# Kernel tuning notes

Measured on AMD Instinct MI355X. Metric: run time of the kernel, lower is better.

Reference implementation:

```python
import jax, jax.numpy as jnp
import numpy as np


def setup_inputs() -> dict:
    key = jax.random.key(0)
    k1, k2 = jax.random.split(key)
    L = 4096000  # 160^3 mesh points
    B = 64       # receivers
    # mesh coordinates in a 10m x 8m x 3m room
    mesh_3D = jax.random.uniform(k1, (L, 3), dtype=jnp.float32) * jnp.array([10.0, 8.0, 3.0], jnp.float32)
    receiver_pos = jax.random.uniform(k2, (B, 3), dtype=jnp.float32) * jnp.array([10.0, 8.0, 3.0], jnp.float32)
    return {"mesh_3D": mesh_3D, "receiver_pos": receiver_pos}


def reference(mesh_3D, receiver_pos):
    # mesh_3D: (L, 3) flattened meshgrid; receiver_pos: (B, 3)
    mesh_flat = mesh_3D.reshape(-1, 3)                      # (L, 3)
    L = mesh_flat.shape[0]
    # Brute-force squared distances via ||m||^2 - 2 m.r + ||r||^2 -> (B, L)
    # (sqrt is monotone, argmin unchanged; distances themselves are not returned)
    m_sq = jnp.sum(mesh_flat * mesh_flat, axis=1)           # (L,)
    r_sq = jnp.sum(receiver_pos * receiver_pos, axis=1)     # (B,)
    cross = receiver_pos @ mesh_flat.T                      # (B, L)
    d2 = m_sq[None, :] - 2.0 * cross + r_sq[:, None]        # (B, L)
    min_idx = jnp.argmin(d2, axis=1)                        # (B,)
    one_hot = jnp.zeros((L,), mesh_flat.dtype).at[min_idx].set(1.0)
    closest_points = mesh_flat[min_idx]                     # (B, 3)
    input_tensor = jnp.concatenate([mesh_flat, one_hot[:, None]], axis=1)  # (L, 4)
    return input_tensor, closest_points
```

## Files before the change

### kernel.cpp

```cpp
#include <hip/hip_runtime.h>
#include <cfloat>
#include <math.h>
#include <stdint.h>

#pragma clang fp contract(off)

#define RPW 16
#define PPL 4
#define NQ  256

__device__ __forceinline__ uint32_t monotone_key(float f) {
    uint32_t u = __float_as_uint(f);
    return (u & 0x80000000u) ? ~u : (u | 0x80000000u);
}

__device__ __forceinline__ float rfl_f(float x) {
    return __uint_as_float((uint32_t)__builtin_amdgcn_readfirstlane((int)__float_as_uint(x)));
}

__global__ void __launch_bounds__(256, 4) fused_kernel(
        const float* __restrict__ mesh, const float* __restrict__ recv,
        float* __restrict__ out, unsigned long long* __restrict__ ws,
        int L, int B, int ntiles) {
    __shared__ unsigned long long lds1[256][RPW + 1];
    __shared__ unsigned long long lds2[16][RPW + 1];

    const int tid  = threadIdx.x;
    const int lane = tid & 63;
    const int wave = tid >> 6;
    const int rq   = blockIdx.x / NQ;
    const int q0   = blockIdx.x % NQ;

    float rx[RPW], ry[RPW], rz[RPW], rsq[RPW];
#pragma unroll
    for (int c = 0; c < RPW; ++c) {
        const int r = rq * RPW + c;
        float x = 0.f, y = 0.f, z = 0.f;
        if (r < B) {
            x = recv[r * 3 + 0];
            y = recv[r * 3 + 1];
            z = recv[r * 3 + 2];
        }
        rx[c]  = rfl_f(x);
        ry[c]  = rfl_f(y);
        rz[c]  = rfl_f(z);
        rsq[c] = rfl_f((x * x + y * y) + z * z);
    }

    float best[RPW];
    int   bidx[RPW];
#pragma unroll
    for (int c = 0; c < RPW; ++c) { best[c] = FLT_MAX; bidx[c] = 0x7fffffff; }

    const bool writer = (rq == 0);

    for (int t = q0; t < ntiles; t += NQ) {
        const int p0 = (t << 10) + (wave << 8) + (lane << 2);
        float xs[PPL], ys[PPL], zs[PPL], ms[PPL];
        if (p0 + PPL <= L) {
            const float4* __restrict__ m4 = (const float4*)(mesh + (size_t)p0 * 3);
            const float4 fa = m4[0], fb = m4[1], fc = m4[2];
            if (writer) {
                float4* __restrict__ o4 = (float4*)(out + (size_t)p0 * 4);
                o4[0] = make_float4(fa.x, fa.y, fa.z, 0.f);
                o4[1] = make_float4(fa.w, fb.x, fb.y, 0.f);
                o4[2] = make_float4(fb.z, fb.w, fc.x, 0.f);
                o4[3] = make_float4(fc.y, fc.z, fc.w, 0.f);
            }
            xs[0] = fa.x; ys[0] = fa.y; zs[0] = fa.z;
            xs[1] = fa.w; ys[1] = fb.x; zs[1] = fb.y;
            xs[2] = fb.z; ys[2] = fb.w; zs[2] = fc.x;
            xs[3] = fc.y; ys[3] = fc.z; zs[3] = fc.w;
#pragma unroll
            for (int j = 0; j < PPL; ++j)
                ms[j] = (xs[j] * xs[j] + ys[j] * ys[j]) + zs[j] * zs[j];
        } else {
#pragma unroll
            for (int j = 0; j < PPL; ++j) {
                const int p = p0 + j;
                if (p < L) {
                    xs[j] = mesh[(size_t)p * 3 + 0];
                    ys[j] = mesh[(size_t)p * 3 + 1];
                    zs[j] = mesh[(size_t)p * 3 + 2];
                    ms[j] = (xs[j] * xs[j] + ys[j] * ys[j]) + zs[j] * zs[j];
                    if (writer) {
                        out[(size_t)p * 4 + 0] = xs[j];
                        out[(size_t)p * 4 + 1] = ys[j];
                        out[(size_t)p * 4 + 2] = zs[j];
                        out[(size_t)p * 4 + 3] = 0.f;
                    }
                } else {
                    xs[j] = 0.f; ys[j] = 0.f; zs[j] = 0.f;
                    ms[j] = INFINITY;
                }
            }
        }
#pragma unroll
        for (int j = 0; j < PPL; ++j) {
            const int gidx = p0 + j;
#pragma unroll
            for (int c = 0; c < RPW; ++c) {
                float cr = fmaf(rz[c], zs[j], fmaf(ry[c], ys[j], rx[c] * xs[j]));
                float d2 = fmaf(-2.0f, cr, ms[j]) + rsq[c];
                if (d2 < best[c]) { best[c] = d2; bidx[c] = gidx; }
            }
        }
    }

#pragma unroll
    for (int c = 0; c < RPW; ++c)
        lds1[tid][c] = ((unsigned long long)monotone_key(best[c]) << 32)
                       | (unsigned int)bidx[c];
    __syncthreads();

    {
        const int c = tid & 15;
        const int g = tid >> 4;
        unsigned long long k = lds1[g * 16][c];
#pragma unroll
        for (int s = 1; s < 16; ++s) {
            unsigned long long o = lds1[g * 16 + s][c];
            if (o < k) k = o;
        }
        lds2[g][c] = k;
    }
    __syncthreads();

    if (tid < RPW) {
        unsigned long long k = lds2[0][tid];
#pragma unroll
        for (int p = 1; p < 16; ++p) {
            unsigned long long o = lds2[p][tid];
            if (o < k) k = o;
        }
        const int r = rq * RPW + tid;
        if (r < B) atomicMin(&ws[r], k);
    }
}

__global__ void finalize_kernel(
        const float* __restrict__ mesh, const unsigned long long* __restrict__ ws,
        float* __restrict__ out, int L, int B) {
    const int r = threadIdx.x;
    if (r >= B) return;
    const int idx = (int)(ws[r] & 0xFFFFFFFFull);
    out[(size_t)idx * 4 + 3] = 1.0f;
    float* cp = out + (size_t)L * 4 + (size_t)r * 3;
    cp[0] = mesh[(size_t)idx * 3 + 0];
    cp[1] = mesh[(size_t)idx * 3 + 1];
    cp[2] = mesh[(size_t)idx * 3 + 2];
}

extern "C" void kernel_launch(void* const* d_in, const int* in_sizes, int n_in,
                              void* d_out, int out_size, void* d_ws, size_t ws_size,
                              hipStream_t stream) {
    const float* mesh = (const float*)d_in[0];
    const float* recv = (const float*)d_in[1];
    float* out = (float*)d_out;
    const int L = in_sizes[0] / 3;
    const int B = in_sizes[1] / 3;
    unsigned long long* ws = (unsigned long long*)d_ws;

    hipMemsetAsync(ws, 0xFF, (size_t)B * sizeof(unsigned long long), stream);

    const int ntiles = (L + 1023) / 1024;
    fused_kernel<<<4 * NQ, 256, 0, stream>>>(mesh, recv, out, ws, L, B, ntiles);

    finalize_kernel<<<1, 64, 0, stream>>>(mesh, ws, out, L, B);
}
```

Baseline: 70.21 us.

## Spread output writes across receiver groups, double grid, shuffle-based block reduction

Doubles the number of tile-parallel blocks and raises the launch-bounds occupancy hint from 4 to 8 blocks per CU. The (L,4) output write is spread across all four receiver-group blocks (each writes the tiles where t mod 4 matches its group) rather than only group 0, which balances store traffic. The large LDS reduction buffer is replaced by a wave-level 64-bit shuffle reduction plus a tiny per-wave LDS array. The higher occupancy target may force register spilling, given the 16-receiver state per thread.

Measured after the change: 147.8 us. +110.6%, slower.

```diff
diff --git a/kernel.cpp b/kernel.cpp
--- a/kernel.cpp
+++ b/kernel.cpp
@@ -6,8 +6,7 @@
 #pragma clang fp contract(off)
 
 #define RPW 16
-#define PPL 4
-#define NQ  256
+#define NQ  512
 
 __device__ __forceinline__ uint32_t monotone_key(float f) {
     uint32_t u = __float_as_uint(f);
@@ -18,12 +17,18 @@
     return __uint_as_float((uint32_t)__builtin_amdgcn_readfirstlane((int)__float_as_uint(x)));
 }
 
-__global__ void __launch_bounds__(256, 4) fused_kernel(
+__device__ __forceinline__ unsigned long long shfl_xor_u64(unsigned long long v, int m) {
+    uint32_t lo = (uint32_t)v, hi = (uint32_t)(v >> 32);
+    lo = (uint32_t)__shfl_xor((int)lo, m, 64);
+    hi = (uint32_t)__shfl_xor((int)hi, m, 64);
+    return ((unsigned long long)hi << 32) | lo;
+}
+
+__global__ void __launch_bounds__(256, 8) fused_kernel(
         const float* __restrict__ mesh, const float* __restrict__ recv,
         float* __restrict__ out, unsigned long long* __restrict__ ws,
         int L, int B, int ntiles) {
-    __shared__ unsigned long long lds1[256][RPW + 1];
-    __shared__ unsigned long long lds2[16][RPW + 1];
+    __shared__ unsigned long long wmin[4][RPW];
 
     const int tid  = threadIdx.x;
     const int lane = tid & 63;
@@ -52,85 +57,67 @@
 #pragma unroll
     for (int c = 0; c < RPW; ++c) { best[c] = FLT_MAX; bidx[c] = 0x7fffffff; }
 
-    const bool writer = (rq == 0);
+    auto eval_point = [&](float x, float y, float z, int gidx) {
+        const float ms = (x * x + y * y) + z * z;
+#pragma unroll
+        for (int c = 0; c < RPW; ++c) {
+            float cr = fmaf(rz[c], z, fmaf(ry[c], y, rx[c] * x));
+            float d2 = fmaf(-2.0f, cr, ms) + rsq[c];
+            if (d2 < best[c]) { best[c] = d2; bidx[c] = gidx; }
+        }
+    };
 
     for (int t = q0; t < ntiles; t += NQ) {
         const int p0 = (t << 10) + (wave << 8) + (lane << 2);
-        float xs[PPL], ys[PPL], zs[PPL], ms[PPL];
-        if (p0 + PPL <= L) {
+        if (p0 + 4 <= L) {
             const float4* __restrict__ m4 = (const float4*)(mesh + (size_t)p0 * 3);
             const float4 fa = m4[0], fb = m4[1], fc = m4[2];
-            if (writer) {
+            if ((t & 3) == rq) {
                 float4* __restrict__ o4 = (float4*)(out + (size_t)p0 * 4);
                 o4[0] = make_float4(fa.x, fa.y, fa.z, 0.f);
                 o4[1] = make_float4(fa.w, fb.x, fb.y, 0.f);
                 o4[2] = make_float4(fb.z, fb.w, fc.x, 0.f);
                 o4[3] = make_float4(fc.y, fc.z, fc.w, 0.f);
             }
-            xs[0] = fa.x; ys[0] = fa.y; zs[0] = fa.z;
-            xs[1] = fa.w; ys[1] = fb.x; zs[1] = fb.y;
-            xs[2] = fb.z; ys[2] = fb.w; zs[2] = fc.x;
-            xs[3] = fc.y; ys[3] = fc.z; zs[3] = fc.w;
-#pragma unroll
-            for (int j = 0; j < PPL; ++j)
-                ms[j] = (xs[j] * xs[j] + ys[j] * ys[j]) + zs[j] * zs[j];
+            eval_point(fa.x, fa.y, fa.z, p0 + 0);
+            eval_point(fa.w, fb.x, fb.y, p0 + 1);
+            eval_point(fb.z, fb.w, fc.x, p0 + 2);
+            eval_point(fc.y, fc.z, fc.w, p0 + 3);
         } else {
-#pragma unroll
-            for (int j = 0; j < PPL; ++j) {
+            for (int j = 0; j < 4; ++j) {
                 const int p = p0 + j;
-                if (p < L) {
-                    xs[j] = mesh[(size_t)p * 3 + 0];
-                    ys[j] = mesh[(size_t)p * 3 + 1];
-                    zs[j] = mesh[(size_t)p * 3 + 2];
-                    ms[j] = (xs[j] * xs[j] + ys[j] * ys[j]) + zs[j] * zs[j];
-                    if (writer) {
-                        out[(size_t)p * 4 + 0] = xs[j];
-                        out[(size_t)p * 4 + 1] = ys[j];
-                        out[(size_t)p * 4 + 2] = zs[j];
-                        out[(size_t)p * 4 + 3] = 0.f;
-                    }
-                } else {
-                    xs[j] = 0.f; ys[j] = 0.f; zs[j] = 0.f;
-                    ms[j] = INFINITY;
+                if (p >= L) break;
+                const float x = mesh[(size_t)p * 3 + 0];
+                const float y = mesh[(size_t)p * 3 + 1];
+                const float z = mesh[(size_t)p * 3 + 2];
+                if ((t & 3) == rq) {
+                    out[(size_t)p * 4 + 0] = x;
+                    out[(size_t)p * 4 + 1] = y;
+                    out[(size_t)p * 4 + 2] = z;
+                    out[(size_t)p * 4 + 3] = 0.f;
                 }
-            }
-        }
-#pragma unroll
-        for (int j = 0; j < PPL; ++j) {
-            const int gidx = p0 + j;
-#pragma unroll
-            for (int c = 0; c < RPW; ++c) {
-                float cr = fmaf(rz[c], zs[j], fmaf(ry[c], ys[j], rx[c] * xs[j]));
-                float d2 = fmaf(-2.0f, cr, ms[j]) + rsq[c];
-                if (d2 < best[c]) { best[c] = d2; bidx[c] = gidx; }
+                eval_point(x, y, z, p);
             }
         }
     }
 
 #pragma unroll
-    for (int c = 0; c < RPW; ++c)
-        lds1[tid][c] = ((unsigned long long)monotone_key(best[c]) << 32)
-                       | (unsigned int)bidx[c];
-    __syncthreads();
-
-    {
-        const int c = tid & 15;
-        const int g = tid >> 4;
-        unsigned long long k = lds1[g * 16][c];
+    for (int c = 0; c < RPW; ++c) {
+        unsigned long long k =
+            ((unsigned long long)monotone_key(best[c]) << 32) | (unsigned int)bidx[c];
 #pragma unroll
-        for (int s = 1; s < 16; ++s) {
-            unsigned long long o = lds1[g * 16 + s][c];
+        for (int off = 32; off >= 1; off >>= 1) {
+            unsigned long long o = shfl_xor_u64(k, off);
             if (o < k) k = o;
         }
-        lds2[g][c] = k;
+        if (lane == 0) wmin[wave][c] = k;
     }
     __syncthreads();
-
     if (tid < RPW) {
-        unsigned long long k = lds2[0][tid];
+        unsigned long long k = wmin[0][tid];
 #pragma unroll
-        for (int p = 1; p < 16; ++p) {
-            unsigned long long o = lds2[p][tid];
+        for (int w = 1; w < 4; ++w) {
+            unsigned long long o = wmin[w][tid];
             if (o < k) k = o;
         }
         const int r = rq * RPW + tid;
```
